# Kernel optimization log

Measured on AMD Instinct MI355X. Metric: run time of the kernel, lower is better.

## Reference

```python
import jax, jax.numpy as jnp
import numpy as np
import math

IN_F = 1024
OUT_F = 1024
B = 16
L = 4096  # img_size (number of positions)


def setup_inputs() -> dict:
    key = jax.random.key(0)
    k1, k2, k3 = jax.random.split(key, 3)
    Efou = jax.random.normal(k1, (B, L, IN_F), dtype=jnp.float32)
    y = jax.random.normal(k2, (B, IN_F), dtype=jnp.float32)
    weight = jax.random.normal(k3, (1, OUT_F, IN_F, 1), dtype=jnp.float32)
    return {"Efou": Efou, "y": y, "weight": weight}


def reference(Efou, y, weight):
    b, img_size, in_f = Efou.shape
    out_f = weight.shape[1]
    scale = 1.0 / math.sqrt(in_f)
    # per-sample modulated weights: [B, out, in]
    w = scale * weight[:, :, :, 0] * y[:, None, :]
    # demodulation norm over the input-feature axis
    dnorm = jax.lax.rsqrt(jnp.sum(w * w, axis=2, keepdims=True) + 1e-8)  # [B, out, 1]
    w = w * dnorm
    # faithful to torch: Efou.reshape(1, B*in, L) is a raw row-major reshape
    E = Efou.reshape(b, in_f, img_size)  # [B, in, L] (same bytes as original)
    x = jnp.einsum('boi,bil->bol', w, E)  # grouped conv1d, kernel size 1
    # faithful to torch: x.view(B, L, out) is a raw reshape of [B, out, L]
    return x.reshape(b, img_size, out_f)
```

## Files before the change

kernel.cpp:

```cpp
#include <hip/hip_runtime.h>
#include <hip/hip_bf16.h>
#include <cstdint>
#include <cstddef>

typedef __bf16 bf16x8 __attribute__((ext_vector_type(8)));
typedef __bf16 bf16x4 __attribute__((ext_vector_type(4)));
typedef float f32x4 __attribute__((ext_vector_type(4)));

#define BATCH 16
#define MDIM 1024
#define NDIM 4096
#define KDIM 1024
#define BM 256
#define BN 256
#define BK 64
#define NKT (KDIM / BK)

__device__ __forceinline__ void gload_lds16(const void* g, void* l) {
  __builtin_amdgcn_global_load_lds(
      (const __attribute__((address_space(1))) void*)g,
      (__attribute__((address_space(3))) void*)l, 16, 0, 0);
}

#define BAR() __builtin_amdgcn_s_barrier()
#define SB() __builtin_amdgcn_sched_barrier(0)
#define FENCE() asm volatile("" ::: "memory")
#define LGKM0()                                        \
  do {                                                 \
    asm volatile("s_waitcnt lgkmcnt(0)" ::: "memory"); \
    SB();                                              \
  } while (0)
#define VMC36()                                        \
  do {                                                 \
    asm volatile("s_waitcnt vmcnt(36)" ::: "memory");  \
    SB();                                              \
  } while (0)

__global__ __launch_bounds__(256) void modw_kernel(
    const float* __restrict__ weight, const float* __restrict__ y,
    __bf16* __restrict__ wm) {
  const int blk = blockIdx.x;
  const int b = blk & 15;
  const int o = blk >> 4;
  const int t = threadIdx.x;
  const float4 w4 = reinterpret_cast<const float4*>(weight + (size_t)o * KDIM)[t];
  const float4 y4 = reinterpret_cast<const float4*>(y + (size_t)b * KDIM)[t];
  const float p0 = w4.x * y4.x, p1 = w4.y * y4.y;
  const float p2 = w4.z * y4.z, p3 = w4.w * y4.w;
  float s = p0 * p0 + p1 * p1 + p2 * p2 + p3 * p3;
#pragma unroll
  for (int off = 32; off >= 1; off >>= 1) s += __shfl_xor(s, off, 64);
  __shared__ float ps[4];
  if ((t & 63) == 0) ps[t >> 6] = s;
  __syncthreads();
  const float tot = ps[0] + ps[1] + ps[2] + ps[3];
  const float scale = 0.03125f;
  const float dn = scale * rsqrtf(scale * scale * tot + 1e-8f);
  bf16x4 v;
  v[0] = (__bf16)(p0 * dn);
  v[1] = (__bf16)(p1 * dn);
  v[2] = (__bf16)(p2 * dn);
  v[3] = (__bf16)(p3 * dn);
  *reinterpret_cast<bf16x4*>(wm + ((size_t)b * MDIM + o) * KDIM + t * 4) = v;
}

__global__ __launch_bounds__(512, 2) void gemm_kernel(
    const __bf16* __restrict__ Wm, const float* __restrict__ E,
    float* __restrict__ out) {
  const int orig = blockIdx.x;
  const int wg = (orig & 7) * 128 + (orig >> 3);
  const int mt = wg & 3;
  const int nt = (wg >> 2) & 15;
  const int b = wg >> 6;
  const int m0 = mt * BM, n0 = nt * BN;

  __shared__ __align__(16) char smem[163840];
  char* const A0_ = smem;
  char* const A1_ = smem + 32768;
  char* const A2_ = smem + 65536;
  char* const B0_ = smem + 98304;
  char* const B1_ = smem + 131072;

  const int tid = threadIdx.x;
  const int lane = tid & 63;
  const int wid = tid >> 6;
  const int wr = wid >> 2;
  const int wc = wid & 3;
  const int ml = lane & 15;
  const int kg = lane >> 4;

  const int arow = tid >> 3;
  const int aswz = ((tid & 7) ^ (arow & 7)) * 8;
  const __bf16* Ag = Wm + ((size_t)(b * MDIM + m0 + arow)) * KDIM + aswz;
  const int aldsOff = tid * 16;

  const int bn1 = tid & 63;
  const int bkg = tid >> 6;
  typedef const __attribute__((address_space(1))) float gfloat;
  gfloat* Eg = (gfloat*)(E + (size_t)b * KDIM * NDIM +
                         (size_t)(bkg * 8) * NDIM + n0 + bn1);
  int bwr[4];
#pragma unroll
  for (int c = 0; c < 4; ++c) {
    const int n = bn1 + 64 * c;
    bwr[c] = n * 128 + ((bkg * 16) ^ ((n & 7) << 4));
  }

  const int colA = (kg * 16) ^ ((ml & 7) << 4);
  const int arB = (wr * 128 + ml) * 128;
  const int brB = (wc * 64 + ml) * 128;

  f32x4 acc[8][4];
#pragma unroll
  for (int i = 0; i < 8; ++i)
#pragma unroll
    for (int j = 0; j < 4; ++j) acc[i][j] = (f32x4){0.f, 0.f, 0.f, 0.f};

  auto stageA = [&](char* Ab, int kt) {
#pragma unroll
    for (int r = 0; r < 4; ++r)
      gload_lds16(Ag + (size_t)(64 * r) * KDIM + kt * BK,
                  Ab + aldsOff + r * 8192);
  };
  auto loadB = [&](float (&brr)[4][8], int kt) {
#pragma unroll
    for (int c = 0; c < 4; ++c)
#pragma unroll
      for (int j = 0; j < 8; ++j)
        brr[c][j] = Eg[(size_t)(kt * BK + j) * NDIM + 64 * c];
  };
  auto writeB = [&](char* Bb, float (&brr)[4][8]) {
#pragma unroll
    for (int c = 0; c < 4; ++c) {
      bf16x8 v;
#pragma unroll
      for (int j = 0; j < 8; ++j) v[j] = (__bf16)brr[c][j];
      *reinterpret_cast<bf16x8*>(Bb + bwr[c]) = v;
    }
  };
  auto rdA = [&](bf16x8 (&d)[4], const char* Ab, int qm, int kk) {
#pragma unroll
    for (int i = 0; i < 4; ++i)
      d[i] = *reinterpret_cast<const bf16x8*>(Ab + arB + (qm * 4 + i) * 2048 +
                                              (colA ^ (kk * 64)));
  };
  auto rdB = [&](bf16x8 (&d)[4], const char* Bb, int kk) {
#pragma unroll
    for (int nf = 0; nf < 4; ++nf)
      d[nf] = *reinterpret_cast<const bf16x8*>(Bb + brB + nf * 2048 +
                                               (colA ^ (kk * 64)));
  };
  auto mfma16 = [&](bf16x8 (&a)[4], bf16x8 (&bv)[4], int qm) {
    __builtin_amdgcn_s_setprio(1);
#pragma unroll
    for (int i = 0; i < 4; ++i)
#pragma unroll
      for (int nf = 0; nf < 4; ++nf)
        acc[qm * 4 + i][nf] = __builtin_amdgcn_mfma_f32_16x16x32_bf16(
            a[i], bv[nf], acc[qm * 4 + i][nf], 0, 0, 0);
    __builtin_amdgcn_s_setprio(0);
  };

  float br[4][8];
  bf16x8 af0[4], af1[4];
  bf16x8 bf0[4], bf1[4];

  {
    float brT[4][8];
    stageA(A0_, 0);
    FENCE();
    loadB(brT, 0);
    writeB(B0_, brT);
    loadB(br, 1);
    FENCE();
    stageA(A1_, 1);
    LGKM0();
    BAR();
    rdA(af0, A0_, 0, 0);
    rdB(bf0, B0_, 0);
  }

  char* Acur = A0_;
  char* Anxt = A1_;
  char* Astg = A2_;
  char* Bc = B0_;
  char* Bo = B1_;

#pragma unroll 1
  for (int t = 0; t < NKT; ++t) {
    const int t2 = (t + 2 < NKT) ? t + 2 : (t + 2 - NKT);

    rdA(af1, Acur, 1, 0);
    writeB(Bo, br);
    mfma16(af0, bf0, 0);

    loadB(br, t2);
    FENCE();
    rdB(bf1, Bc, 1);
    rdA(af0, Acur, 0, 1);
    stageA(Astg, t2);
    mfma16(af1, bf0, 1);

    rdA(af1, Acur, 1, 1);
    mfma16(af0, bf1, 0);
    LGKM0();
    VMC36();
    BAR();

    rdA(af0, Anxt, 0, 0);
    rdB(bf0, Bo, 0);
    mfma16(af1, bf1, 1);

    char* ta = Acur; Acur = Anxt; Anxt = Astg; Astg = ta;
    char* tb = Bc; Bc = Bo; Bo = tb;
  }

  float* ob = out + ((size_t)(b * MDIM + m0 + wr * 128 + kg * 4)) * NDIM +
              n0 + wc * 64 + ml;
#pragma unroll
  for (int mf = 0; mf < 8; ++mf)
#pragma unroll
    for (int nf = 0; nf < 4; ++nf) {
      const f32x4 a = acc[mf][nf];
      float* p = ob + (size_t)mf * 16 * NDIM + nf * 16;
#pragma unroll
      for (int q = 0; q < 4; ++q) p[(size_t)q * NDIM] = a[q];
    }
}

extern "C" void kernel_launch(void* const* d_in, const int* in_sizes, int n_in,
                              void* d_out, int out_size, void* d_ws,
                              size_t ws_size, hipStream_t stream) {
  (void)in_sizes;
  (void)n_in;
  (void)out_size;
  (void)ws_size;
  const float* Efou = (const float*)d_in[0];
  const float* y = (const float*)d_in[1];
  const float* weight = (const float*)d_in[2];
  float* outp = (float*)d_out;
  __bf16* wm = (__bf16*)d_ws;

  modw_kernel<<<dim3(BATCH * MDIM), dim3(256), 0, stream>>>(weight, y, wm);
  gemm_kernel<<<dim3(BATCH * (MDIM / BM) * (NDIM / BN)), dim3(512), 0,
                stream>>>(wm, Efou, outp);
}
```

Baseline: 212.5 us.

## Loop each GEMM block over all M tiles for one batch/N tile

The grid shrinks from 1024 to 256 workgroups. Each workgroup now walks the four M tiles of a fixed (batch, N-tile) pair in one flattened loop, storing and resetting its accumulators after every 16 K-steps. The aim is to keep the E column panel hot in cache across M tiles, cut launch and tail overhead, and free LDS by moving A from triple to double buffering. The cost is one workgroup per CU instead of two, and A is now prefetched only one step ahead, so latency hiding may suffer.

```diff
diff --git a/kernel.cpp b/kernel.cpp
--- a/kernel.cpp
+++ b/kernel.cpp
@@ -15,6 +15,8 @@
 #define BN 256
 #define BK 64
 #define NKT (KDIM / BK)
+#define NPASS 4
+#define NG (NKT * NPASS)
 
 __device__ __forceinline__ void gload_lds16(const void* g, void* l) {
   __builtin_amdgcn_global_load_lds(
@@ -30,9 +32,9 @@
     asm volatile("s_waitcnt lgkmcnt(0)" ::: "memory"); \
     SB();                                              \
   } while (0)
-#define VMC36()                                        \
+#define VMC32()                                        \
   do {                                                 \
-    asm volatile("s_waitcnt vmcnt(36)" ::: "memory");  \
+    asm volatile("s_waitcnt vmcnt(32)" ::: "memory");  \
     SB();                                              \
   } while (0)
 
@@ -67,19 +69,16 @@
 __global__ __launch_bounds__(512, 2) void gemm_kernel(
     const __bf16* __restrict__ Wm, const float* __restrict__ E,
     float* __restrict__ out) {
-  const int orig = blockIdx.x;
-  const int wg = (orig & 7) * 128 + (orig >> 3);
-  const int mt = wg & 3;
-  const int nt = (wg >> 2) & 15;
-  const int b = wg >> 6;
-  const int m0 = mt * BM, n0 = nt * BN;
-
-  __shared__ __align__(16) char smem[163840];
+  const int blk = blockIdx.x;
+  const int nt = blk & 15;
+  const int b = blk >> 4;
+  const int n0 = nt * BN;
+
+  __shared__ __align__(16) char smem[131072];
   char* const A0_ = smem;
   char* const A1_ = smem + 32768;
-  char* const A2_ = smem + 65536;
-  char* const B0_ = smem + 98304;
-  char* const B1_ = smem + 131072;
+  char* const B0_ = smem + 65536;
+  char* const B1_ = smem + 98304;
 
   const int tid = threadIdx.x;
   const int lane = tid & 63;
@@ -91,7 +90,7 @@
 
   const int arow = tid >> 3;
   const int aswz = ((tid & 7) ^ (arow & 7)) * 8;
-  const __bf16* Ag = Wm + ((size_t)(b * MDIM + m0 + arow)) * KDIM + aswz;
+  const __bf16* Ag = Wm + ((size_t)(b * MDIM + arow)) * KDIM + aswz;
   const int aldsOff = tid * 16;
 
   const int bn1 = tid & 63;
@@ -116,13 +115,16 @@
 #pragma unroll
     for (int j = 0; j < 4; ++j) acc[i][j] = (f32x4){0.f, 0.f, 0.f, 0.f};
 
-  auto stageA = [&](char* Ab, int kt) {
+  auto stageA = [&](char* Ab, int g) {
+    const int moff = ((g >> 4) & 3) * BM;
+    const int kt = g & 15;
 #pragma unroll
     for (int r = 0; r < 4; ++r)
-      gload_lds16(Ag + (size_t)(64 * r) * KDIM + kt * BK,
+      gload_lds16(Ag + (size_t)(moff + 64 * r) * KDIM + kt * BK,
                   Ab + aldsOff + r * 8192);
   };
-  auto loadB = [&](float (&brr)[4][8], int kt) {
+  auto loadB = [&](float (&brr)[4][8], int g) {
+    const int kt = g & 15;
 #pragma unroll
     for (int c = 0; c < 4; ++c)
 #pragma unroll
@@ -172,8 +174,6 @@
     loadB(brT, 0);
     writeB(B0_, brT);
     loadB(br, 1);
-    FENCE();
-    stageA(A1_, 1);
     LGKM0();
     BAR();
     rdA(af0, A0_, 0, 0);
@@ -181,51 +181,59 @@
   }
 
   char* Acur = A0_;
-  char* Anxt = A1_;
-  char* Astg = A2_;
+  char* Ao = A1_;
   char* Bc = B0_;
   char* Bo = B1_;
 
 #pragma unroll 1
-  for (int t = 0; t < NKT; ++t) {
-    const int t2 = (t + 2 < NKT) ? t + 2 : (t + 2 - NKT);
+  for (int g = 0; g < NG; ++g) {
+    const int g1 = (g + 1) & (NG - 1);
+    const int g2 = (g + 2) & (NG - 1);
 
     rdA(af1, Acur, 1, 0);
     writeB(Bo, br);
     mfma16(af0, bf0, 0);
 
-    loadB(br, t2);
-    FENCE();
     rdB(bf1, Bc, 1);
     rdA(af0, Acur, 0, 1);
-    stageA(Astg, t2);
+    stageA(Ao, g1);
+    FENCE();
+    loadB(br, g2);
     mfma16(af1, bf0, 1);
 
     rdA(af1, Acur, 1, 1);
     mfma16(af0, bf1, 0);
     LGKM0();
-    VMC36();
+    VMC32();
     BAR();
 
-    rdA(af0, Anxt, 0, 0);
+    rdA(af0, Ao, 0, 0);
     rdB(bf0, Bo, 0);
     mfma16(af1, bf1, 1);
 
-    char* ta = Acur; Acur = Anxt; Anxt = Astg; Astg = ta;
+    if ((g & 15) == 15) {
+      const int mt = g >> 4;
+      float* ob = out +
+                  ((size_t)(b * MDIM + mt * BM + wr * 128 + kg * 4)) * NDIM +
+                  n0 + wc * 64 + ml;
+#pragma unroll
+      for (int mf = 0; mf < 8; ++mf)
+#pragma unroll
+        for (int nf = 0; nf < 4; ++nf) {
+          const f32x4 a = acc[mf][nf];
+          float* p = ob + (size_t)mf * 16 * NDIM + nf * 16;
+#pragma unroll
+          for (int q = 0; q < 4; ++q) p[(size_t)q * NDIM] = a[q];
+        }
+#pragma unroll
+      for (int i = 0; i < 8; ++i)
+#pragma unroll
+        for (int j = 0; j < 4; ++j) acc[i][j] = (f32x4){0.f, 0.f, 0.f, 0.f};
+    }
+
+    char* ta = Acur; Acur = Ao; Ao = ta;
     char* tb = Bc; Bc = Bo; Bo = tb;
   }
-
-  float* ob = out + ((size_t)(b * MDIM + m0 + wr * 128 + kg * 4)) * NDIM +
-              n0 + wc * 64 + ml;
-#pragma unroll
-  for (int mf = 0; mf < 8; ++mf)
-#pragma unroll
-    for (int nf = 0; nf < 4; ++nf) {
-      const f32x4 a = acc[mf][nf];
-      float* p = ob + (size_t)mf * 16 * NDIM + nf * 16;
-#pragma unroll
-      for (int q = 0; q < 4; ++q) p[(size_t)q * NDIM] = a[q];
-    }
 }
 
 extern "C" void kernel_launch(void* const* d_in, const int* in_sizes, int n_in,
@@ -242,6 +250,6 @@
   __bf16* wm = (__bf16*)d_ws;
 
   modw_kernel<<<dim3(BATCH * MDIM), dim3(256), 0, stream>>>(weight, y, wm);
-  gemm_kernel<<<dim3(BATCH * (MDIM / BM) * (NDIM / BN)), dim3(512), 0,
-                stream>>>(wm, Efou, outp);
-}
+  gemm_kernel<<<dim3(BATCH * (NDIM / BN)), dim3(512), 0, stream>>>(wm, Efou,
+                                                                   outp);
+}
```

Result: slower. 297.4 us (+39.9%).
